# Performance work log

Hardware: AMD Instinct MI355X
Metric: run time of the kernel (lower is better)

The kernel has to match this reference:

```python
import jax, jax.numpy as jnp
import numpy as np

L, B, T, D, H = 12, 8, 512, 768, 12
DH = D // H
EPS = 1e-12


def _layernorm(x, w, b):
    u = jnp.mean(x, axis=-1, keepdims=True)
    s = jnp.mean(jnp.square(x - u), axis=-1, keepdims=True)
    return w * ((x - u) / jnp.sqrt(s + EPS)) + b


def setup_inputs() -> dict:
    key = jax.random.key(0)
    ks = jax.random.split(key, 8)
    w = lambda k: jax.random.normal(k, (L, D, D), dtype=jnp.float32) * 0.02
    return {
        "query_states": jax.random.normal(ks[0], (B, T, D), dtype=jnp.float32),
        "hidden_states": jax.random.normal(ks[1], (B, T, D), dtype=jnp.float32),
        "attention_mask": jnp.zeros((B, 1, 1, T), dtype=jnp.float32),
        "Wq": w(ks[2]), "bq": jnp.zeros((L, D), jnp.float32),
        "Wk": w(ks[3]), "bk": jnp.zeros((L, D), jnp.float32),
        "Wv": w(ks[4]), "bv": jnp.zeros((L, D), jnp.float32),
        "Wo1": w(ks[5]), "bo1": jnp.zeros((L, D), jnp.float32),
        "ln1_w": jnp.ones((L, D), jnp.float32), "ln1_b": jnp.zeros((L, D), jnp.float32),
        "Wo2": w(ks[6]), "bo2": jnp.zeros((L, D), jnp.float32),
        "ln2_w": jnp.ones((L, D), jnp.float32), "ln2_b": jnp.zeros((L, D), jnp.float32),
    }


def reference(query_states, hidden_states, attention_mask,
              Wq, bq, Wk, bk, Wv, bv,
              Wo1, bo1, ln1_w, ln1_b,
              Wo2, bo2, ln2_w, ln2_b):
    scale = 1.0 / jnp.sqrt(jnp.float32(DH))

    def heads(x):  # [B,T,D] -> [B,H,T,DH]
        return x.reshape(B, T, H, DH).transpose(0, 2, 1, 3)

    def layer_fn(hidden, p):
        (wq, bq_, wk, bk_, wv, bv_, wo1, bo1_, l1w, l1b, wo2, bo2_, l2w, l2b) = p
        q = heads(query_states @ wq + bq_)
        k = heads(hidden @ wk + bk_)
        v = heads(hidden @ wv + bv_)
        scores = jnp.einsum("bhqd,bhkd->bhqk", q, k) * scale + attention_mask
        probs = jax.nn.softmax(scores, axis=-1)
        ctx = jnp.einsum("bhqk,bhkd->bhqd", probs, v)
        ctx = ctx.transpose(0, 2, 1, 3).reshape(B, T, D)
        # attention Output: LN(dense(ctx) + key_states)
        attn_out = _layernorm(ctx @ wo1 + bo1_ + hidden, l1w, l1b)
        # layer Output (intermediate is identity in source): LN(dense(attn_out) + attn_out)
        out = _layernorm(attn_out @ wo2 + bo2_ + attn_out, l2w, l2b)
        return out, None

    params = (Wq, bq, Wk, bk, Wv, bv, Wo1, bo1, ln1_w, ln1_b, Wo2, bo2, ln2_w, ln2_b)
    hidden, _ = jax.lax.scan(layer_fn, hidden_states, params)
    return hidden
```

## Files before the change

kernel.cpp:

```cpp
#include <hip/hip_runtime.h>
#include <stdint.h>

#define L_ 12
#define B_ 8
#define T_ 512
#define D_ 768
#define H_ 12
#define DH_ 64
#define M_ 4096
#define DD_ (D_*D_)

typedef unsigned short u16;
typedef __bf16 bf16x8 __attribute__((ext_vector_type(8)));
typedef float f32x4 __attribute__((ext_vector_type(4)));
typedef u16 u16x4 __attribute__((ext_vector_type(4)));
typedef u16 u16x8 __attribute__((ext_vector_type(8)));

static __device__ __forceinline__ u16 f2b(float f) {
  union { float f; unsigned u; } x; x.f = f;
  unsigned r = x.u + 0x7fffu + ((x.u >> 16) & 1u);
  return (u16)(r >> 16);
}
static __device__ __forceinline__ float b2f(u16 u) {
  union { unsigned u; float f; } x; x.u = ((unsigned)u) << 16; return x.f;
}
static __device__ __forceinline__ void gload16(u16* lds, const u16* g) {
  __builtin_amdgcn_global_load_lds((__attribute__((address_space(1))) void*)(g),
                                   (__attribute__((address_space(3))) void*)(lds), 16, 0, 0);
}
static __device__ __forceinline__ f32x4 mfma16(bf16x8 a, bf16x8 b, f32x4 c) {
  return __builtin_amdgcn_mfma_f32_16x16x32_bf16(a, b, c, 0, 0, 0);
}
static __device__ __forceinline__ bf16x8 ldfrag(const u16* p) {
  return *reinterpret_cast<const bf16x8*>(p);
}

__global__ void init_kernel(const float* __restrict__ qs, const float* __restrict__ hs,
                            u16* __restrict__ qsb, u16* __restrict__ hidb, int n) {
  int i = blockIdx.x * 256 + threadIdx.x;
  if (i < n) {
    qsb[i] = f2b(qs[i]);
    hidb[i] = f2b(hs[i]);
  }
}

__global__ void wt_kernel(const float* W0, const float* W1, const float* W2,
                          const float* W3, const float* W4, u16* __restrict__ out) {
  const int z = blockIdx.z, layer = z / 5, w = z % 5;
  const float* base = (w == 0) ? W0 : (w == 1) ? W1 : (w == 2) ? W2 : (w == 3) ? W3 : W4;
  const float* W = base + (size_t)layer * DD_;
  u16* O = out + (size_t)z * DD_;
  const int nb = blockIdx.x * 64, kb = blockIdx.y * 64;
  __shared__ u16 tile[64][66];
  const int tid = threadIdx.x;
  #pragma unroll
  for (int p = 0; p < 4; ++p) {
    const int idx = p * 256 + tid;
    const int kr = idx >> 4, n4 = (idx & 15) * 4;
    const f32x4 v4 = *reinterpret_cast<const f32x4*>(W + (size_t)(kb + kr) * D_ + nb + n4);
    #pragma unroll
    for (int i = 0; i < 4; i++) tile[n4 + i][kr] = f2b(v4[i]);
  }
  __syncthreads();
  #pragma unroll
  for (int p = 0; p < 4; ++p) {
    const int idx = p * 256 + tid;
    const int n = idx >> 4, k4 = (idx & 15) * 4;
    u16x4 o4;
    #pragma unroll
    for (int i = 0; i < 4; i++) o4[i] = tile[n][k4 + i];
    *reinterpret_cast<u16x4*>(O + (size_t)(nb + n) * D_ + kb + k4) = o4;
  }
}

static __device__ void gemm_core(const u16* __restrict__ A, const u16* __restrict__ W,
                                 const float* __restrict__ bias, const u16* __restrict__ resb,
                                 float* __restrict__ outf, u16* __restrict__ outb) {
  __shared__ __align__(16) u16 lA[2][64 * 64];
  __shared__ __align__(16) u16 lB[2][128 * 64];
  const int tid = threadIdx.x;
  const int wave = tid >> 6, lane = tid & 63;
  const int wm = wave >> 1, wn = wave & 1;

  const int nbx = gridDim.x;
  const int nwg = nbx * gridDim.y;
  const int orig = blockIdx.y * nbx + blockIdx.x;
  const int cpx = nwg >> 3;
  const int swz = (orig & 7) * cpx + (orig >> 3);
  const int m0 = (swz / nbx) * 64, n0 = (swz % nbx) * 128;
  const int lr = lane & 15, lg = lane >> 4;

  f32x4 acc[2][4];
  #pragma unroll
  for (int i = 0; i < 2; i++)
    #pragma unroll
    for (int j = 0; j < 4; j++) acc[i][j] = f32x4{0.f, 0.f, 0.f, 0.f};

  const int uA0 = wave * 64 + lane, uA1 = 256 + uA0;
  const int rA0 = uA0 >> 3, cA0 = ((uA0 & 7) ^ (rA0 & 7)) << 3;
  const int rA1 = uA1 >> 3, cA1 = ((uA1 & 7) ^ (rA1 & 7)) << 3;
  const u16* Ab0 = A + (size_t)(m0 + rA0) * D_ + cA0;
  const u16* Ab1 = A + (size_t)(m0 + rA1) * D_ + cA1;
  const u16* Wb[4];
  #pragma unroll
  for (int q = 0; q < 4; ++q) {
    const int u = q * 256 + wave * 64 + lane;
    const int r = u >> 3, c = ((u & 7) ^ (r & 7)) << 3;
    Wb[q] = W + (size_t)(n0 + r) * D_ + c;
  }

#define STAGE(buf, k0_) do {                                   \
    gload16(lA[buf] + wave * 512,        Ab0 + (k0_));         \
    gload16(lA[buf] + 2048 + wave * 512, Ab1 + (k0_));         \
    gload16(lB[buf] + wave * 512,        Wb[0] + (k0_));       \
    gload16(lB[buf] + 2048 + wave * 512, Wb[1] + (k0_));       \
    gload16(lB[buf] + 4096 + wave * 512, Wb[2] + (k0_));       \
    gload16(lB[buf] + 6144 + wave * 512, Wb[3] + (k0_));       \
  } while (0)

  STAGE(0, 0);
  __syncthreads();

  const int sx = lr & 7;

  int cur = 0;
  for (int kt = 0; kt < 12; ++kt) {
    if (kt < 11) STAGE(cur ^ 1, (kt + 1) * 64);
    bf16x8 af[2][2], bw[2][4];
    #pragma unroll
    for (int kk = 0; kk < 2; ++kk) {
      const int uo = ((kk * 4 + lg) ^ sx) << 3;
      #pragma unroll
      for (int i = 0; i < 2; i++)
        af[kk][i] = ldfrag(lA[cur] + ((wm * 32 + i * 16 + lr) << 6) + uo);
      #pragma unroll
      for (int j = 0; j < 4; j++)
        bw[kk][j] = ldfrag(lB[cur] + ((wn * 64 + j * 16 + lr) << 6) + uo);
    }
    #pragma unroll
    for (int kk = 0; kk < 2; ++kk)
      #pragma unroll
      for (int i = 0; i < 2; i++)
        #pragma unroll
        for (int j = 0; j < 4; j++)
          acc[i][j] = mfma16(af[kk][i], bw[kk][j], acc[i][j]);
    __syncthreads();
    cur ^= 1;
  }
#undef STAGE

  #pragma unroll
  for (int j = 0; j < 4; j++) {
    const int colg = n0 + wn * 64 + j * 16 + lr;
    const float bv = bias[colg];
    #pragma unroll
    for (int i = 0; i < 2; i++) {
      const int rowb = m0 + wm * 32 + i * 16 + lg * 4;
      #pragma unroll
      for (int r = 0; r < 4; r++) {
        float v = acc[i][j][r] + bv;
        const size_t off = (size_t)(rowb + r) * D_ + colg;
        if (resb) v += b2f(resb[off]);
        if (outf) outf[off] = v;
        if (outb) outb[off] = f2b(v);
      }
    }
  }
}

__global__ __launch_bounds__(256) void qkv_kernel(
    const u16* qsb, const u16* hidb,
    const u16* wq, const u16* wk, const u16* wv,
    const float* bq, const float* bk, const float* bv,
    u16* q, u16* k, u16* v) {
  const u16* A; const u16* W; const float* bias; u16* out;
  if (blockIdx.z == 0)      { A = qsb;  W = wq; bias = bq; out = q; }
  else if (blockIdx.z == 1) { A = hidb; W = wk; bias = bk; out = k; }
  else                      { A = hidb; W = wv; bias = bv; out = v; }
  gemm_core(A, W, bias, nullptr, nullptr, out);
}

__global__ __launch_bounds__(256) void o_kernel(const u16* A, const u16* W, const float* bias,
                                                const u16* resb, float* outf) {
  gemm_core(A, W, bias, resb, outf, nullptr);
}

__global__ void vtrans_kernel(const u16* __restrict__ v, u16* __restrict__ vt) {
  const int bh = blockIdx.y, b = bh / H_, h = bh % H_;
  const int t0 = blockIdx.x * 64;
  __shared__ u16 tile[64][66];
  const int tid = threadIdx.x;
  #pragma unroll
  for (int p = 0; p < 2; ++p) {
    const int idx = p * 256 + tid;
    const int r = idx >> 3, c8 = (idx & 7) * 8;
    const u16x8 v8 = *reinterpret_cast<const u16x8*>(
        v + (size_t)(b * T_ + t0 + r) * D_ + h * DH_ + c8);
    #pragma unroll
    for (int i = 0; i < 8; i++) tile[c8 + i][r] = v8[i];
  }
  __syncthreads();
  #pragma unroll
  for (int p = 0; p < 2; ++p) {
    const int idx = p * 256 + tid;
    const int dh = idx >> 3, k8 = (idx & 7) * 8;
    u16x8 o8;
    #pragma unroll
    for (int i = 0; i < 8; i++) o8[i] = tile[dh][k8 + i];
    *reinterpret_cast<u16x8*>(vt + ((size_t)bh * DH_ + dh) * T_ + t0 + k8) = o8;
  }
}

__global__ __launch_bounds__(256) void attn_kernel(const u16* __restrict__ q, const u16* __restrict__ k,
                                                   const u16* __restrict__ vt, const float* __restrict__ mask,
                                                   u16* __restrict__ ctx) {
  __shared__ __align__(16) u16 KT[2][64 * 64];
  __shared__ __align__(16) u16 VT[2][64 * 64];
  __shared__ __align__(16) u16 PT[4 * 16 * 64];
  const int tid = threadIdx.x, wave = tid >> 6, lane = tid & 63;
  const int id = blockIdx.x;
  const int bh = id % 96, qblk = id / 96;
  const int b = bh / H_, h = bh % H_;
  const int q0 = qblk * 64 + wave * 16;
  const int lr = lane & 15, lg = lane >> 4;

  bf16x8 qa0, qa1;
  {
    const u16* qp = q + (size_t)(b * T_ + q0 + lr) * D_ + h * DH_ + lg * 8;
    qa0 = ldfrag(qp);
    qa1 = ldfrag(qp + 32);
  }

  const int su0 = wave * 64 + lane, su1 = 256 + wave * 64 + lane;
  const int sr0 = su0 >> 3, sc0 = ((su0 & 7) ^ (sr0 & 7)) << 3;
  const int sr1 = su1 >> 3, sc1 = ((su1 & 7) ^ (sr1 & 7)) << 3;
  const u16* kbase = k + (size_t)b * T_ * D_ + h * DH_;
  const u16* vbase = vt + (size_t)bh * DH_ * T_;

#define STAGEKV(buf, kt_) do {                                                         \
    gload16(KT[buf] + wave * 512,        kbase + (size_t)((kt_) * 64 + sr0) * D_ + sc0); \
    gload16(KT[buf] + 2048 + wave * 512, kbase + (size_t)((kt_) * 64 + sr1) * D_ + sc1); \
    gload16(VT[buf] + wave * 512,        vbase + (size_t)sr0 * T_ + (kt_) * 64 + sc0);   \
    gload16(VT[buf] + 2048 + wave * 512, vbase + (size_t)sr1 * T_ + (kt_) * 64 + sc1);   \
  } while (0)

  float mrow[4] = {-1e30f, -1e30f, -1e30f, -1e30f};
  float lrow[4] = {0.f, 0.f, 0.f, 0.f};
  f32x4 O[4] = { {0,0,0,0}, {0,0,0,0}, {0,0,0,0}, {0,0,0,0} };
  u16* Pw = PT + wave * 1024;

  STAGEKV(0, 0);
  int cur = 0;
  for (int kt = 0; kt < 8; ++kt) {
    __syncthreads();
    if (kt < 7) STAGEKV(cur ^ 1, kt + 1);

    f32x4 S[4];
    #pragma unroll
    for (int nf = 0; nf < 4; ++nf) {
      const u16* kr = KT[cur] + (nf * 16 + lr) * 64;
      bf16x8 kb0 = ldfrag(kr + ((lg       ^ (lr & 7)) << 3));
      bf16x8 kb1 = ldfrag(kr + (((4 + lg) ^ (lr & 7)) << 3));
      f32x4 a = {0.f, 0.f, 0.f, 0.f};
      a = mfma16(qa0, kb0, a);
      a = mfma16(qa1, kb1, a);
      S[nf] = a;
    }
    #pragma unroll
    for (int nf = 0; nf < 4; ++nf) {
      const float mk = mask[(size_t)b * T_ + kt * 64 + nf * 16 + lr];
      #pragma unroll
      for (int r = 0; r < 4; r++) S[nf][r] = S[nf][r] * 0.125f + mk;
    }
    #pragma unroll
    for (int r = 0; r < 4; r++) {
      float tm = fmaxf(fmaxf(S[0][r], S[1][r]), fmaxf(S[2][r], S[3][r]));
      #pragma unroll
      for (int d = 1; d <= 8; d <<= 1) tm = fmaxf(tm, __shfl_xor(tm, d));
      const float mn = fmaxf(mrow[r], tm);
      const float sc = __expf(mrow[r] - mn);
      float ts = 0.f;
      #pragma unroll
      for (int nf = 0; nf < 4; ++nf) { float pv = __expf(S[nf][r] - mn); S[nf][r] = pv; ts += pv; }
      #pragma unroll
      for (int d = 1; d <= 8; d <<= 1) ts += __shfl_xor(ts, d);
      lrow[r] = lrow[r] * sc + ts;
      mrow[r] = mn;
      #pragma unroll
      for (int nf = 0; nf < 4; ++nf) O[nf][r] *= sc;
    }
    #pragma unroll
    for (int nf = 0; nf < 4; ++nf)
      #pragma unroll
      for (int r = 0; r < 4; r++) {
        const int R = lg * 4 + r;
        Pw[R * 64 + ((((nf << 1) | (lr >> 3)) ^ (R & 7)) << 3) + (lr & 7)] = f2b(S[nf][r]);
      }
    #pragma unroll
    for (int ks = 0; ks < 2; ++ks) {
      bf16x8 pa = ldfrag(Pw + lr * 64 + (((ks * 4 + lg) ^ (lr & 7)) << 3));
      #pragma unroll
      for (int nf = 0; nf < 4; ++nf) {
        bf16x8 vb = ldfrag(VT[cur] + (nf * 16 + lr) * 64 + (((ks * 4 + lg) ^ (lr & 7)) << 3));
        O[nf] = mfma16(pa, vb, O[nf]);
      }
    }
    cur ^= 1;
  }
#undef STAGEKV

  #pragma unroll
  for (int r = 0; r < 4; r++) {
    const float inv = 1.f / lrow[r];
    const int row = q0 + lg * 4 + r;
    #pragma unroll
    for (int nf = 0; nf < 4; ++nf)
      ctx[(size_t)(b * T_ + row) * D_ + h * DH_ + nf * 16 + lr] = f2b(O[nf][r] * inv);
  }
}

__global__ __launch_bounds__(256) void ln_kernel(const float* __restrict__ y,
                                                 const float* __restrict__ w, const float* __restrict__ bp,
                                                 float* __restrict__ outf, u16* __restrict__ outb) {
  const int wave = threadIdx.x >> 6, lane = threadIdx.x & 63;
  const int row = blockIdx.x * 4 + wave;
  const f32x4* yp = (const f32x4*)(y + (size_t)row * D_);
  f32x4 x[3];
  #pragma unroll
  for (int j = 0; j < 3; j++) x[j] = yp[j * 64 + lane];
  float s = 0.f;
  #pragma unroll
  for (int j = 0; j < 3; j++) s += x[j][0] + x[j][1] + x[j][2] + x[j][3];
  #pragma unroll
  for (int d = 1; d <= 32; d <<= 1) s += __shfl_xor(s, d);
  const float u = s * (1.f / D_);
  float v = 0.f;
  #pragma unroll
  for (int j = 0; j < 3; j++)
    #pragma unroll
    for (int c = 0; c < 4; c++) { float t = x[j][c] - u; v += t * t; }
  #pragma unroll
  for (int d = 1; d <= 32; d <<= 1) v += __shfl_xor(v, d);
  const float rinv = rsqrtf(v * (1.f / D_) + 1e-12f);
  const f32x4* wp = (const f32x4*)w;
  const f32x4* bpp = (const f32x4*)bp;
  #pragma unroll
  for (int j = 0; j < 3; j++) {
    const f32x4 w4 = wp[j * 64 + lane];
    const f32x4 b4 = bpp[j * 64 + lane];
    f32x4 o4;
    u16x4 ob;
    #pragma unroll
    for (int c = 0; c < 4; c++) {
      o4[c] = w4[c] * ((x[j][c] - u) * rinv) + b4[c];
      ob[c] = f2b(o4[c]);
    }
    if (outf) ((f32x4*)(outf + (size_t)row * D_))[j * 64 + lane] = o4;
    ((u16x4*)(outb + (size_t)row * D_))[j * 64 + lane] = ob;
  }
}

extern "C" void kernel_launch(void* const* d_in, const int* in_sizes, int n_in,
                              void* d_out, int out_size, void* d_ws, size_t ws_size,
                              hipStream_t stream) {
  const float* qs   = (const float*)d_in[0];
  const float* hs   = (const float*)d_in[1];
  const float* mask = (const float*)d_in[2];
  const float* Wq   = (const float*)d_in[3];
  const float* bq   = (const float*)d_in[4];
  const float* Wk   = (const float*)d_in[5];
  const float* bk   = (const float*)d_in[6];
  const float* Wv   = (const float*)d_in[7];
  const float* bv   = (const float*)d_in[8];
  const float* Wo1  = (const float*)d_in[9];
  const float* bo1  = (const float*)d_in[10];
  const float* l1w  = (const float*)d_in[11];
  const float* l1b  = (const float*)d_in[12];
  const float* Wo2  = (const float*)d_in[13];
  const float* bo2  = (const float*)d_in[14];
  const float* l2w  = (const float*)d_in[15];
  const float* l2b  = (const float*)d_in[16];
  float* out = (float*)d_out;

  char* p = (char*)d_ws;
  auto alloc = [&](size_t bytes) { char* r = p; p += (bytes + 255) & ~(size_t)255; return r; };
  u16*   qsb  = (u16*)alloc((size_t)M_ * D_ * 2);
  u16*   hidb = (u16*)alloc((size_t)M_ * D_ * 2);
  u16*   qb   = (u16*)alloc((size_t)M_ * D_ * 2);
  u16*   kb_  = (u16*)alloc((size_t)M_ * D_ * 2);
  u16*   vb_  = (u16*)alloc((size_t)M_ * D_ * 2);
  u16*   vtb  = (u16*)alloc((size_t)M_ * D_ * 2);
  u16*   ctxb = (u16*)alloc((size_t)M_ * D_ * 2);
  float* y    = (float*)alloc((size_t)M_ * D_ * 4);
  u16*   aob  = (u16*)alloc((size_t)M_ * D_ * 2);
  const size_t base_used = (size_t)(p - (char*)d_ws);
  const size_t full_wt_bytes = (size_t)60 * DD_ * 2;
  const bool wt_once = (ws_size - base_used) >= full_wt_bytes + 256;
  u16* wt60 = (u16*)alloc(wt_once ? full_wt_bytes : (size_t)5 * DD_ * 2);

  init_kernel<<<(M_ * D_ + 255) / 256, 256, 0, stream>>>(qs, hs, qsb, hidb, M_ * D_);
  if (wt_once)
    wt_kernel<<<dim3(12, 12, 60), 256, 0, stream>>>(Wq, Wk, Wv, Wo1, Wo2, wt60);

  for (int l = 0; l < L_; ++l) {
    const size_t wo = (size_t)l * DD_;
    u16* wt = wt_once ? (wt60 + (size_t)l * 5 * DD_) : wt60;
    if (!wt_once)
      wt_kernel<<<dim3(12, 12, 5), 256, 0, stream>>>(Wq + wo, Wk + wo, Wv + wo, Wo1 + wo, Wo2 + wo, wt);
    qkv_kernel<<<dim3(6, 64, 3), 256, 0, stream>>>(qsb, hidb,
        wt, wt + DD_, wt + 2 * DD_, bq + l * D_, bk + l * D_, bv + l * D_, qb, kb_, vb_);
    vtrans_kernel<<<dim3(8, 96), 256, 0, stream>>>(vb_, vtb);
    attn_kernel<<<768, 256, 0, stream>>>(qb, kb_, vtb, mask, ctxb);
    o_kernel<<<dim3(6, 64), 256, 0, stream>>>(ctxb, wt + 3 * DD_, bo1 + l * D_, hidb, y);
    ln_kernel<<<1024, 256, 0, stream>>>(y, l1w + l * D_, l1b + l * D_, nullptr, aob);
    o_kernel<<<dim3(6, 64), 256, 0, stream>>>(aob, wt + 4 * DD_, bo2 + l * D_, aob, y);
    ln_kernel<<<1024, 256, 0, stream>>>(y, l2w + l * D_, l2b + l * D_,
                                        (l == L_ - 1) ? out : nullptr, hidb);
  }
}
```

Measured before the change: 1.375 ms.

## Write V transposed from GEMM epilogue and hoist Q projections for all layers

The V projection GEMM now writes its output directly in the per-head transposed layout, which removes the separate vtrans kernel and its extra global round trip. Because query_states does not change across layers, the Q projections for all 12 layers are computed up front in one large batched launch into a new workspace buffer. Each layer then only runs the K/V GEMMs. This cuts per-layer launches and increases parallelism, at the cost of a large extra workspace allocation and strided 8-byte stores in the V epilogue.

Measured after the change: 1.326 ms. -3.6%, faster.

```diff
diff --git a/kernel.cpp b/kernel.cpp
--- a/kernel.cpp
+++ b/kernel.cpp
@@ -75,7 +75,8 @@
 
 static __device__ void gemm_core(const u16* __restrict__ A, const u16* __restrict__ W,
                                  const float* __restrict__ bias, const u16* __restrict__ resb,
-                                 float* __restrict__ outf, u16* __restrict__ outb) {
+                                 float* __restrict__ outf, u16* __restrict__ outb,
+                                 u16* __restrict__ outv) {
   __shared__ __align__(16) u16 lA[2][64 * 64];
   __shared__ __align__(16) u16 lB[2][128 * 64];
   const int tid = threadIdx.x;
@@ -149,6 +150,24 @@
   }
 #undef STAGE
 
+  if (outv) {
+    #pragma unroll
+    for (int j = 0; j < 4; j++) {
+      const int colg = n0 + wn * 64 + j * 16 + lr;
+      const float bv = bias[colg];
+      const int h = colg >> 6, dh = colg & 63;
+      #pragma unroll
+      for (int i = 0; i < 2; i++) {
+        const int rowb = m0 + wm * 32 + i * 16 + lg * 4;
+        const int bb = rowb >> 9, t = rowb & 511;
+        u16x4 o4;
+        #pragma unroll
+        for (int r = 0; r < 4; r++) o4[r] = f2b(acc[i][j][r] + bv);
+        *reinterpret_cast<u16x4*>(outv + ((size_t)((bb * H_ + h) * DH_ + dh)) * T_ + t) = o4;
+      }
+    }
+    return;
+  }
   #pragma unroll
   for (int j = 0; j < 4; j++) {
     const int colg = n0 + wn * 64 + j * 16 + lr;
@@ -168,47 +187,33 @@
   }
 }
 
-__global__ __launch_bounds__(256) void qkv_kernel(
-    const u16* qsb, const u16* hidb,
-    const u16* wq, const u16* wk, const u16* wv,
-    const float* bq, const float* bk, const float* bv,
-    u16* q, u16* k, u16* v) {
-  const u16* A; const u16* W; const float* bias; u16* out;
-  if (blockIdx.z == 0)      { A = qsb;  W = wq; bias = bq; out = q; }
-  else if (blockIdx.z == 1) { A = hidb; W = wk; bias = bk; out = k; }
-  else                      { A = hidb; W = wv; bias = bv; out = v; }
-  gemm_core(A, W, bias, nullptr, nullptr, out);
+__global__ __launch_bounds__(256) void qall_kernel(const u16* qsb, const u16* wt60,
+                                                   const float* bq, u16* qall) {
+  const int l = blockIdx.z;
+  gemm_core(qsb, wt60 + (size_t)l * 5 * DD_, bq + l * D_, nullptr,
+            nullptr, qall + (size_t)l * M_ * D_, nullptr);
+}
+
+__global__ __launch_bounds__(256) void kv_kernel(const u16* hidb,
+                                                 const u16* wk, const u16* wv,
+                                                 const float* bk, const float* bv,
+                                                 u16* kout, u16* vtout) {
+  if (blockIdx.z == 0) gemm_core(hidb, wk, bk, nullptr, nullptr, kout, nullptr);
+  else                 gemm_core(hidb, wv, bv, nullptr, nullptr, nullptr, vtout);
+}
+
+__global__ __launch_bounds__(256) void qkv3_kernel(const u16* qsb, const u16* hidb,
+                                                   const u16* wq, const u16* wk, const u16* wv,
+                                                   const float* bq, const float* bk, const float* bv,
+                                                   u16* q, u16* kout, u16* vtout) {
+  if (blockIdx.z == 0)      gemm_core(qsb,  wq, bq, nullptr, nullptr, q, nullptr);
+  else if (blockIdx.z == 1) gemm_core(hidb, wk, bk, nullptr, nullptr, kout, nullptr);
+  else                      gemm_core(hidb, wv, bv, nullptr, nullptr, nullptr, vtout);
 }
 
 __global__ __launch_bounds__(256) void o_kernel(const u16* A, const u16* W, const float* bias,
                                                 const u16* resb, float* outf) {
-  gemm_core(A, W, bias, resb, outf, nullptr);
-}
-
-__global__ void vtrans_kernel(const u16* __restrict__ v, u16* __restrict__ vt) {
-  const int bh = blockIdx.y, b = bh / H_, h = bh % H_;
-  const int t0 = blockIdx.x * 64;
-  __shared__ u16 tile[64][66];
-  const int tid = threadIdx.x;
-  #pragma unroll
-  for (int p = 0; p < 2; ++p) {
-    const int idx = p * 256 + tid;
-    const int r = idx >> 3, c8 = (idx & 7) * 8;
-    const u16x8 v8 = *reinterpret_cast<const u16x8*>(
-        v + (size_t)(b * T_ + t0 + r) * D_ + h * DH_ + c8);
-    #pragma unroll
-    for (int i = 0; i < 8; i++) tile[c8 + i][r] = v8[i];
-  }
-  __syncthreads();
-  #pragma unroll
-  for (int p = 0; p < 2; ++p) {
-    const int idx = p * 256 + tid;
-    const int dh = idx >> 3, k8 = (idx & 7) * 8;
-    u16x8 o8;
-    #pragma unroll
-    for (int i = 0; i < 8; i++) o8[i] = tile[dh][k8 + i];
-    *reinterpret_cast<u16x8*>(vt + ((size_t)bh * DH_ + dh) * T_ + t0 + k8) = o8;
-  }
+  gemm_core(A, W, bias, resb, outf, nullptr, nullptr);
 }
 
 __global__ __launch_bounds__(256) void attn_kernel(const u16* __restrict__ q, const u16* __restrict__ k,
@@ -386,31 +391,43 @@
   auto alloc = [&](size_t bytes) { char* r = p; p += (bytes + 255) & ~(size_t)255; return r; };
   u16*   qsb  = (u16*)alloc((size_t)M_ * D_ * 2);
   u16*   hidb = (u16*)alloc((size_t)M_ * D_ * 2);
-  u16*   qb   = (u16*)alloc((size_t)M_ * D_ * 2);
   u16*   kb_  = (u16*)alloc((size_t)M_ * D_ * 2);
-  u16*   vb_  = (u16*)alloc((size_t)M_ * D_ * 2);
   u16*   vtb  = (u16*)alloc((size_t)M_ * D_ * 2);
   u16*   ctxb = (u16*)alloc((size_t)M_ * D_ * 2);
   float* y    = (float*)alloc((size_t)M_ * D_ * 4);
   u16*   aob  = (u16*)alloc((size_t)M_ * D_ * 2);
+  u16*   qb   = (u16*)alloc((size_t)M_ * D_ * 2);
   const size_t base_used = (size_t)(p - (char*)d_ws);
-  const size_t full_wt_bytes = (size_t)60 * DD_ * 2;
-  const bool wt_once = (ws_size - base_used) >= full_wt_bytes + 256;
-  u16* wt60 = (u16*)alloc(wt_once ? full_wt_bytes : (size_t)5 * DD_ * 2);
+  const size_t wt60_bytes = (size_t)60 * DD_ * 2;
+  const size_t qall_bytes = (size_t)12 * M_ * D_ * 2;
+  const bool wt_once  = (ws_size - base_used) >= wt60_bytes + 512;
+  u16* wt60 = (u16*)alloc(wt_once ? wt60_bytes : (size_t)5 * DD_ * 2);
+  const size_t used2 = (size_t)(p - (char*)d_ws);
+  const bool q_all   = wt_once && (ws_size - used2) >= qall_bytes + 512;
+  u16* qall = q_all ? (u16*)alloc(qall_bytes) : qb;
 
   init_kernel<<<(M_ * D_ + 255) / 256, 256, 0, stream>>>(qs, hs, qsb, hidb, M_ * D_);
   if (wt_once)
     wt_kernel<<<dim3(12, 12, 60), 256, 0, stream>>>(Wq, Wk, Wv, Wo1, Wo2, wt60);
+  if (q_all)
+    qall_kernel<<<dim3(6, 64, 12), 256, 0, stream>>>(qsb, wt60, bq, qall);
 
   for (int l = 0; l < L_; ++l) {
     const size_t wo = (size_t)l * DD_;
     u16* wt = wt_once ? (wt60 + (size_t)l * 5 * DD_) : wt60;
     if (!wt_once)
       wt_kernel<<<dim3(12, 12, 5), 256, 0, stream>>>(Wq + wo, Wk + wo, Wv + wo, Wo1 + wo, Wo2 + wo, wt);
-    qkv_kernel<<<dim3(6, 64, 3), 256, 0, stream>>>(qsb, hidb,
-        wt, wt + DD_, wt + 2 * DD_, bq + l * D_, bk + l * D_, bv + l * D_, qb, kb_, vb_);
-    vtrans_kernel<<<dim3(8, 96), 256, 0, stream>>>(vb_, vtb);
-    attn_kernel<<<768, 256, 0, stream>>>(qb, kb_, vtb, mask, ctxb);
+    const u16* qcur;
+    if (q_all) {
+      qcur = qall + (size_t)l * M_ * D_;
+      kv_kernel<<<dim3(6, 64, 2), 256, 0, stream>>>(hidb, wt + DD_, wt + 2 * DD_,
+                                                    bk + l * D_, bv + l * D_, kb_, vtb);
+    } else {
+      qcur = qb;
+      qkv3_kernel<<<dim3(6, 64, 3), 256, 0, stream>>>(qsb, hidb,
+          wt, wt + DD_, wt + 2 * DD_, bq + l * D_, bk + l * D_, bv + l * D_, qb, kb_, vtb);
+    }
+    attn_kernel<<<768, 256, 0, stream>>>(qcur, kb_, vtb, mask, ctxb);
     o_kernel<<<dim3(6, 64), 256, 0, stream>>>(ctxb, wt + 3 * DD_, bo1 + l * D_, hidb, y);
     ln_kernel<<<1024, 256, 0, stream>>>(y, l1w + l * D_, l1b + l * D_, nullptr, aob);
     o_kernel<<<dim3(6, 64), 256, 0, stream>>>(aob, wt + 4 * DD_, bo2 + l * D_, aob, y);
```
